# Performance work log

Hardware: AMD Instinct MI355X
Metric: run time of the kernel (lower is better)

The kernel has to match this reference:

```python
import jax, jax.numpy as jnp
import numpy as np

RATIO = 1.0 / 32  # spacial_ratio
HOUT = 7          # pooled_h
WOUT = 7          # pooled_w
S = 2             # sub_bin_size = int(sqrt(n_sampled=4))


def setup_inputs() -> dict:
    key = jax.random.key(0)
    k1, k2, k3, k4, k5, k6 = jax.random.split(key, 6)
    B, C, H, W = 4, 256, 50, 50
    N = 1024
    img_w, img_h = W / RATIO, H / RATIO
    features = jax.random.normal(k1, (B, C, H, W), dtype=jnp.float32)
    b = jax.random.randint(k2, (N,), 0, B).astype(jnp.float32)
    x1 = jax.random.uniform(k3, (N,), minval=0.0, maxval=img_w - 232.0)
    y1 = jax.random.uniform(k4, (N,), minval=0.0, maxval=img_h - 232.0)
    bw = jax.random.uniform(k5, (N,), minval=32.0, maxval=232.0)
    bh = jax.random.uniform(k6, (N,), minval=32.0, maxval=232.0)
    rois = jnp.stack([b, x1, y1, x1 + bw, y1 + bh], axis=1)  # [N, 5]
    return {"features": features, "rois": rois}


def _roi_align(features, rois):
    B, C, H, W = features.shape
    fW = jnp.float32(W)
    fH = jnp.float32(H)
    b_idx = rois[:, 0].astype(jnp.int32)            # [N]
    box = rois[:, 1:] * RATIO                       # [N, 4] in feature coords
    bx1 = jnp.clip(box[:, 0], 0.0, fW)
    by1 = jnp.clip(box[:, 1], 0.0, fH)
    bx2 = jnp.clip(box[:, 2], 0.0, fW)
    by2 = jnp.clip(box[:, 3], 0.0, fH)
    roi_valid = (bx2 - bx1 > 0) & (by2 - by1 > 0)   # [N]
    bin_w = (bx2 - bx1) / WOUT                      # [N]
    bin_h = (by2 - by1) / HOUT

    jj = jnp.arange(WOUT, dtype=jnp.float32)
    ii = jnp.arange(HOUT, dtype=jnp.float32)
    # bin edges; y2/x2 computed from the UNclamped start, then clamped (matches original order)
    x1u = bx1[:, None] + jj * bin_w[:, None]        # [N, WOUT]
    x2b = jnp.clip(x1u + bin_w[:, None], 0.0, fW)
    x1b = jnp.clip(x1u, 0.0, fW)
    y1u = by1[:, None] + ii * bin_h[:, None]        # [N, HOUT]
    y2b = jnp.clip(y1u + bin_h[:, None], 0.0, fH)
    y1b = jnp.clip(y1u, 0.0, fH)
    bin_valid = (y2b > y1b)[:, :, None] & (x2b > x1b)[:, None, :]  # [N, HOUT, WOUT]

    # SxS sample-point centers inside each bin (sub_bin = bin / S, center offset 0.5)
    cc = jnp.arange(S, dtype=jnp.float32) + 0.5
    px = x1b[:, :, None] + cc * (bin_w / S)[:, None, None]  # [N, WOUT, S]
    py = y1b[:, :, None] + cc * (bin_h / S)[:, None, None]  # [N, HOUT, S]

    xl = jnp.clip(jnp.floor(px), 0, W - 1).astype(jnp.int32)
    xh = jnp.clip(xl + 1, 0, W - 1)
    yl = jnp.clip(jnp.floor(py), 0, H - 1).astype(jnp.int32)
    yh = jnp.clip(yl + 1, 0, H - 1)
    wxh = px - xl  # (x - x1)
    wxl = xh - px  # (x2 - x)
    wyb = py - yl  # (y - y1)
    wyt = yh - py  # (y2 - y)

    feats = features.transpose(0, 2, 3, 1)          # [B, H, W, C]
    bI = b_idx[:, None, None, None, None]           # [N,1,1,1,1]
    # x varies over (WOUT, sx) -> broadcast axes (2,4); y over (HOUT, sy) -> axes (1,3)
    XL = xl[:, None, :, None, :]
    XH = xh[:, None, :, None, :]
    YL = yl[:, :, None, :, None]
    YH = yh[:, :, None, :, None]
    WXh = wxh[:, None, :, None, :, None]
    WXl = wxl[:, None, :, None, :, None]
    WYb = wyb[:, :, None, :, None, None]
    WYt = wyt[:, :, None, :, None, None]

    v_tl = feats[bI, YL, XL]   # [N, HOUT, WOUT, S, S, C]
    v_tr = feats[bI, YL, XH]
    v_bl = feats[bI, YH, XL]
    v_br = feats[bI, YH, XH]
    top = WXh * v_tr + WXl * v_tl
    bot = WXh * v_br + WXl * v_bl
    val = WYb * bot + WYt * top                     # [N, HOUT, WOUT, S, S, C]

    pooled = val.max(axis=(3, 4))                   # max over sample grid -> [N, HOUT, WOUT, C]
    mask = bin_valid & roi_valid[:, None, None]
    pooled = jnp.where(mask[..., None], pooled, 0.0)
    return pooled.transpose(0, 3, 1, 2)             # [N, C, HOUT, WOUT]


def reference(features, rois):
    return _roi_align(features, rois)
```

## Files before the change

### kernel.cpp

```cpp
#include <hip/hip_runtime.h>


namespace {

constexpr int B_ = 4, C_ = 256, H_ = 50, W_ = 50;
constexpr int HW = H_ * W_;
constexpr int HO = 7, WO = 7, NBIN = HO * WO;
constexpr int OUT_PER_ROI = C_ * NBIN;
constexpr int CPB = 128;
constexpr int COLS = CPB / 4;
constexpr int LDs = 132;
constexpr float RATIO = 1.0f / 32.0f;

__global__ __launch_bounds__(256) void transpose_tiled(
    const float* __restrict__ f, float* __restrict__ ft)
{
    __shared__ float tile[64][65];
    const int bt   = blockIdx.x;
    const int hw_t = bt % 40;
    const int c_t  = (bt / 40) % 4;
    const int b    = bt / 160;
    const int hw0 = hw_t * 64, c0 = c_t * 64;
    const int lx = threadIdx.x & 63;
    const int ly = threadIdx.x >> 6;

#pragma unroll
    for (int k = 0; k < 16; ++k) {
        const int c  = c0 + k * 4 + ly;
        const int hw = hw0 + lx;
        if (hw < HW)
            tile[k * 4 + ly][lx] = f[((size_t)b * C_ + c) * HW + hw];
    }
    __syncthreads();
#pragma unroll
    for (int k = 0; k < 16; ++k) {
        const int hw = hw0 + k * 4 + ly;
        if (hw < HW)
            ft[((size_t)b * HW + hw) * C_ + c0 + lx] = tile[lx][k * 4 + ly];
    }
}

__global__ __launch_bounds__(256, 5) void roialign_main(
    const float* __restrict__ ft,
    const float* __restrict__ rois,
    float* __restrict__ out)
{
    __shared__ float stage[NBIN * LDs];
    __shared__ __align__(16) float    wts[NBIN][8];
    __shared__ __align__(16) unsigned offs[NBIN][8];

    const int n    = blockIdx.x;
    const int half = blockIdx.y;
    const int tid  = threadIdx.x;
    const int wave = tid >> 6;
    const int lane = tid & 63;
    const int col  = lane & 31;
    const int sub  = lane >> 5;
    const float fW = (float)W_, fH = (float)H_;

    if (tid < NBIN) {
        const int ii = tid / WO, jj = tid % WO;
        const float* r = rois + n * 5;
        const float bx1 = fminf(fmaxf(r[1] * RATIO, 0.0f), fW);
        const float by1 = fminf(fmaxf(r[2] * RATIO, 0.0f), fH);
        const float bx2 = fminf(fmaxf(r[3] * RATIO, 0.0f), fW);
        const float by2 = fminf(fmaxf(r[4] * RATIO, 0.0f), fH);
        const bool roi_valid = (bx2 - bx1 > 0.0f) && (by2 - by1 > 0.0f);
        const float bin_w = (bx2 - bx1) * (1.0f / (float)WO);
        const float bin_h = (by2 - by1) * (1.0f / (float)HO);

        const float x1u = bx1 + (float)jj * bin_w;
        const float x1b = fminf(fmaxf(x1u, 0.0f), fW);
        const float x2b = fminf(fmaxf(x1u + bin_w, 0.0f), fW);
        const float y1u = by1 + (float)ii * bin_h;
        const float y1b = fminf(fmaxf(y1u, 0.0f), fH);
        const float y2b = fminf(fmaxf(y1u + bin_h, 0.0f), fH);
        const float vf = (roi_valid && (y2b > y1b) && (x2b > x1b)) ? 1.0f : 0.0f;

        int xl[2], xh[2], yl[2], yh[2];
#pragma unroll
        for (int s = 0; s < 2; ++s) {
            const float px = x1b + ((float)s + 0.5f) * (bin_w * 0.5f);
            int l = (int)floorf(px);
            l = min(max(l, 0), W_ - 1);
            const int h = min(l + 1, W_ - 1);
            xl[s] = l; xh[s] = h;
            wts[tid][0 + s] = vf * (px - (float)l);
            wts[tid][2 + s] = vf * ((float)h - px);

            const float py = y1b + ((float)s + 0.5f) * (bin_h * 0.5f);
            int t = (int)floorf(py);
            t = min(max(t, 0), H_ - 1);
            const int u = min(t + 1, H_ - 1);
            yl[s] = t; yh[s] = u;
            wts[tid][4 + s] = py - (float)t;
            wts[tid][6 + s] = (float)u - py;
        }
#pragma unroll
        for (int sy = 0; sy < 2; ++sy) {
#pragma unroll
            for (int sx = 0; sx < 2; ++sx) {
                const int s = sy * 2 + sx;
                const unsigned tl = (unsigned)(yl[sy] * W_ + xl[sx]);
                const unsigned tr = (unsigned)(yl[sy] * W_ + xh[sx]);
                const unsigned bl = (unsigned)(yh[sy] * W_ + xl[sx]);
                const unsigned br = (unsigned)(yh[sy] * W_ + xh[sx]);
                offs[tid][s * 2 + 0] = tl | (tr << 16);
                offs[tid][s * 2 + 1] = bl | (br << 16);
            }
        }
    }
    __syncthreads();

    int b = (int)rois[n * 5];
    b = min(max(b, 0), B_ - 1);
    const float4* pb = (const float4*)(ft + (size_t)b * HW * C_) + half * COLS + col;

    for (int i0 = wave * 2; i0 < NBIN; i0 += 8) {
        const int bin = i0 + sub;
        const int bc  = min(bin, NBIN - 1);
        const float4 wa = *(const float4*)wts[bc];
        const float4 wb = *(const float4*)(wts[bc] + 4);
        const uint4  oa = *(const uint4*)&offs[bc][0];
        const uint4  ob = *(const uint4*)&offs[bc][4];

        auto samp = [&](unsigned ptop, unsigned pbot,
                        float wxh, float wxl, float wyb, float wyt) -> float4 {
            const int tl = (int)(ptop & 0xffffu) << 6;
            const int tr = (int)(ptop >> 16) << 6;
            const int bl = (int)(pbot & 0xffffu) << 6;
            const int br = (int)(pbot >> 16) << 6;
            const float4 v_tl = pb[tl], v_tr = pb[tr];
            const float4 v_bl = pb[bl], v_br = pb[br];
            float4 o;
            o.x = wyb * (wxh * v_br.x + wxl * v_bl.x) + wyt * (wxh * v_tr.x + wxl * v_tl.x);
            o.y = wyb * (wxh * v_br.y + wxl * v_bl.y) + wyt * (wxh * v_tr.y + wxl * v_tl.y);
            o.z = wyb * (wxh * v_br.z + wxl * v_bl.z) + wyt * (wxh * v_tr.z + wxl * v_tl.z);
            o.w = wyb * (wxh * v_br.w + wxl * v_bl.w) + wyt * (wxh * v_tr.w + wxl * v_tl.w);
            return o;
        };

        const float4 s0 = samp(oa.x, oa.y, wa.x, wa.z, wb.x, wb.z);
        const float4 s1 = samp(oa.z, oa.w, wa.y, wa.w, wb.x, wb.z);
        const float4 s2 = samp(ob.x, ob.y, wa.x, wa.z, wb.y, wb.w);
        const float4 s3 = samp(ob.z, ob.w, wa.y, wa.w, wb.y, wb.w);
        float4 m;
        m.x = fmaxf(fmaxf(s0.x, s1.x), fmaxf(s2.x, s3.x));
        m.y = fmaxf(fmaxf(s0.y, s1.y), fmaxf(s2.y, s3.y));
        m.z = fmaxf(fmaxf(s0.z, s1.z), fmaxf(s2.z, s3.z));
        m.w = fmaxf(fmaxf(s0.w, s1.w), fmaxf(s2.w, s3.w));

        if (bin < NBIN)
            *(float4*)&stage[bin * LDs + 4 * col] = m;
    }
    __syncthreads();

    float* outn = out + (size_t)n * OUT_PER_ROI + half * (CPB * NBIN);
    for (int k = tid; k < CPB * NBIN; k += 256) {
        const int ch = k / NBIN;
        const int bi = k - ch * NBIN;
        outn[k] = stage[bi * LDs + ch];
    }
}

}

extern "C" void kernel_launch(void* const* d_in, const int* in_sizes, int n_in,
                              void* d_out, int out_size, void* d_ws, size_t ws_size,
                              hipStream_t stream)
{
    const float* feats = (const float*)d_in[0];
    const float* rois  = (const float*)d_in[1];
    float* out = (float*)d_out;
    const int N = in_sizes[1] / 5;
    float* ft = (float*)d_ws;

    hipLaunchKernelGGL(transpose_tiled, dim3(B_ * 4 * 40), dim3(256), 0, stream,
                       feats, ft);
    hipLaunchKernelGGL(roialign_main, dim3(N, 2), dim3(256), 0, stream,
                       ft, rois, out);
}
```

Measured before the change: 105.0 us.

## Vectorize transpose with float4 and issue two bins' gathers before computing

The transpose kernel now reads and writes float4 vectors through the shared tile instead of scalar elements. The main kernel's bin loop is restructured so each wave issues all 16 gather loads for two bins before doing any interpolation math, raising memory-level parallelism. Occupancy hint is lowered from 5 to 4 blocks per CU to accommodate the extra registers for 32 in-flight float4 loads. The float4 transpose reads may hit LDS bank conflicts on the column-strided tile accesses.

```diff
diff --git a/kernel.cpp b/kernel.cpp
--- a/kernel.cpp
+++ b/kernel.cpp
@@ -21,26 +21,38 @@
     const int c_t  = (bt / 40) % 4;
     const int b    = bt / 160;
     const int hw0 = hw_t * 64, c0 = c_t * 64;
-    const int lx = threadIdx.x & 63;
-    const int ly = threadIdx.x >> 6;
-
-#pragma unroll
-    for (int k = 0; k < 16; ++k) {
-        const int c  = c0 + k * 4 + ly;
-        const int hw = hw0 + lx;
-        if (hw < HW)
-            tile[k * 4 + ly][lx] = f[((size_t)b * C_ + c) * HW + hw];
+    const int x4 = threadIdx.x & 15;
+    const int cr = threadIdx.x >> 4;
+
+#pragma unroll
+    for (int p = 0; p < 4; ++p) {
+        const int ch = p * 16 + cr;
+        const int hw = hw0 + x4 * 4;
+        if (hw < HW) {
+            const float4 v = *(const float4*)&f[((size_t)(b * C_ + c0 + ch)) * HW + hw];
+            tile[ch][x4 * 4 + 0] = v.x;
+            tile[ch][x4 * 4 + 1] = v.y;
+            tile[ch][x4 * 4 + 2] = v.z;
+            tile[ch][x4 * 4 + 3] = v.w;
+        }
     }
     __syncthreads();
 #pragma unroll
-    for (int k = 0; k < 16; ++k) {
-        const int hw = hw0 + k * 4 + ly;
-        if (hw < HW)
-            ft[((size_t)b * HW + hw) * C_ + c0 + lx] = tile[lx][k * 4 + ly];
-    }
-}
-
-__global__ __launch_bounds__(256, 5) void roialign_main(
+    for (int p = 0; p < 4; ++p) {
+        const int hwr = p * 16 + cr;
+        const int hw  = hw0 + hwr;
+        if (hw < HW) {
+            float4 v;
+            v.x = tile[x4 * 4 + 0][hwr];
+            v.y = tile[x4 * 4 + 1][hwr];
+            v.z = tile[x4 * 4 + 2][hwr];
+            v.w = tile[x4 * 4 + 3][hwr];
+            *(float4*)&ft[((size_t)b * HW + hw) * C_ + c0 + x4 * 4] = v;
+        }
+    }
+}
+
+__global__ __launch_bounds__(256, 4) void roialign_main(
     const float* __restrict__ ft,
     const float* __restrict__ rois,
     float* __restrict__ out)
@@ -116,42 +128,67 @@
     b = min(max(b, 0), B_ - 1);
     const float4* pb = (const float4*)(ft + (size_t)b * HW * C_) + half * COLS + col;
 
-    for (int i0 = wave * 2; i0 < NBIN; i0 += 8) {
-        const int bin = i0 + sub;
-        const int bc  = min(bin, NBIN - 1);
-        const float4 wa = *(const float4*)wts[bc];
-        const float4 wb = *(const float4*)(wts[bc] + 4);
-        const uint4  oa = *(const uint4*)&offs[bc][0];
-        const uint4  ob = *(const uint4*)&offs[bc][4];
-
-        auto samp = [&](unsigned ptop, unsigned pbot,
-                        float wxh, float wxl, float wyb, float wyt) -> float4 {
-            const int tl = (int)(ptop & 0xffffu) << 6;
-            const int tr = (int)(ptop >> 16) << 6;
-            const int bl = (int)(pbot & 0xffffu) << 6;
-            const int br = (int)(pbot >> 16) << 6;
-            const float4 v_tl = pb[tl], v_tr = pb[tr];
-            const float4 v_bl = pb[bl], v_br = pb[br];
+    struct Meta { float4 wa, wb; uint4 oa, ob; int bin; };
+    auto read_meta = [&](int i0) -> Meta {
+        Meta m;
+        m.bin = i0 + sub;
+        const int bc = min(m.bin, NBIN - 1);
+        m.wa = *(const float4*)wts[bc];
+        m.wb = *(const float4*)(wts[bc] + 4);
+        m.oa = *(const uint4*)&offs[bc][0];
+        m.ob = *(const uint4*)&offs[bc][4];
+        return m;
+    };
+    auto issue_loads = [&](const Meta& mt, float4 L[16]) {
+        const unsigned o[8] = { mt.oa.x, mt.oa.y, mt.oa.z, mt.oa.w,
+                                mt.ob.x, mt.ob.y, mt.ob.z, mt.ob.w };
+#pragma unroll
+        for (int s = 0; s < 4; ++s) {
+            const unsigned pt = o[2 * s], pbm = o[2 * s + 1];
+            L[4 * s + 0] = pb[(int)(pt  & 0xffffu) << 6];
+            L[4 * s + 1] = pb[(int)(pt  >> 16)     << 6];
+            L[4 * s + 2] = pb[(int)(pbm & 0xffffu) << 6];
+            L[4 * s + 3] = pb[(int)(pbm >> 16)     << 6];
+        }
+    };
+    auto compute_stage = [&](const Meta& mt, const float4 L[16]) {
+        float4 s4[4];
+#pragma unroll
+        for (int s = 0; s < 4; ++s) {
+            const int sx = s & 1, sy = s >> 1;
+            const float wxh = sx ? mt.wa.y : mt.wa.x;
+            const float wxl = sx ? mt.wa.w : mt.wa.z;
+            const float wyb = sy ? mt.wb.y : mt.wb.x;
+            const float wyt = sy ? mt.wb.w : mt.wb.z;
+            const float4 tl = L[4 * s + 0], tr = L[4 * s + 1];
+            const float4 bl = L[4 * s + 2], br = L[4 * s + 3];
             float4 o;
-            o.x = wyb * (wxh * v_br.x + wxl * v_bl.x) + wyt * (wxh * v_tr.x + wxl * v_tl.x);
-            o.y = wyb * (wxh * v_br.y + wxl * v_bl.y) + wyt * (wxh * v_tr.y + wxl * v_tl.y);
-            o.z = wyb * (wxh * v_br.z + wxl * v_bl.z) + wyt * (wxh * v_tr.z + wxl * v_tl.z);
-            o.w = wyb * (wxh * v_br.w + wxl * v_bl.w) + wyt * (wxh * v_tr.w + wxl * v_tl.w);
-            return o;
-        };
-
-        const float4 s0 = samp(oa.x, oa.y, wa.x, wa.z, wb.x, wb.z);
-        const float4 s1 = samp(oa.z, oa.w, wa.y, wa.w, wb.x, wb.z);
-        const float4 s2 = samp(ob.x, ob.y, wa.x, wa.z, wb.y, wb.w);
-        const float4 s3 = samp(ob.z, ob.w, wa.y, wa.w, wb.y, wb.w);
+            o.x = wyb * (wxh * br.x + wxl * bl.x) + wyt * (wxh * tr.x + wxl * tl.x);
+            o.y = wyb * (wxh * br.y + wxl * bl.y) + wyt * (wxh * tr.y + wxl * tl.y);
+            o.z = wyb * (wxh * br.z + wxl * bl.z) + wyt * (wxh * tr.z + wxl * tl.z);
+            o.w = wyb * (wxh * br.w + wxl * bl.w) + wyt * (wxh * tr.w + wxl * tl.w);
+            s4[s] = o;
+        }
         float4 m;
-        m.x = fmaxf(fmaxf(s0.x, s1.x), fmaxf(s2.x, s3.x));
-        m.y = fmaxf(fmaxf(s0.y, s1.y), fmaxf(s2.y, s3.y));
-        m.z = fmaxf(fmaxf(s0.z, s1.z), fmaxf(s2.z, s3.z));
-        m.w = fmaxf(fmaxf(s0.w, s1.w), fmaxf(s2.w, s3.w));
-
-        if (bin < NBIN)
-            *(float4*)&stage[bin * LDs + 4 * col] = m;
+        m.x = fmaxf(fmaxf(s4[0].x, s4[1].x), fmaxf(s4[2].x, s4[3].x));
+        m.y = fmaxf(fmaxf(s4[0].y, s4[1].y), fmaxf(s4[2].y, s4[3].y));
+        m.z = fmaxf(fmaxf(s4[0].z, s4[1].z), fmaxf(s4[2].z, s4[3].z));
+        m.w = fmaxf(fmaxf(s4[0].w, s4[1].w), fmaxf(s4[2].w, s4[3].w));
+        if (mt.bin < NBIN)
+            *(float4*)&stage[mt.bin * LDs + 4 * col] = m;
+    };
+
+    for (int i0 = wave * 2; i0 < NBIN; i0 += 16) {
+        const int iB = i0 + 8;
+        const bool hasB = (iB < NBIN);
+        Meta mA = read_meta(i0);
+        float4 LA[16];
+        issue_loads(mA, LA);
+        Meta mB;
+        float4 LB[16];
+        if (hasB) { mB = read_meta(iB); issue_loads(mB, LB); }
+        compute_stage(mA, LA);
+        if (hasB) compute_stage(mB, LB);
     }
     __syncthreads();
 
```

Result: slower. 150.1 us (+43.0%).
